# Kernel optimization log

Measured on AMD Instinct MI355X. Metric: run time of the kernel, lower is better.

The kernel has to match this reference:

```python
import jax, jax.numpy as jnp
import numpy as np

N, E = 20000, 160000
NFEAT, NHID, NCLASS = 512, 256, 64


def _unif(key, shape):
    s = 1.0 / np.sqrt(shape[-1])
    return jax.random.uniform(key, shape, jnp.float32, -s, s)


def setup_inputs() -> dict:
    key = jax.random.key(0)
    ks = jax.random.split(key, 16)
    return {
        "x": jax.random.normal(ks[0], (N, NFEAT), jnp.float32),
        "edge_index": jax.random.randint(ks[1], (2, E), 0, N, dtype=jnp.int32).astype(jnp.int64),
        "head": 0,
        # Relation 1 (nfeat -> nfeat)
        "r1_g1": _unif(ks[2], (NFEAT, NFEAT)),
        "r1_g2": _unif(ks[3], (NFEAT, NFEAT)),
        "r1_b1": _unif(ks[4], (NFEAT, NFEAT)),
        "r1_b2": _unif(ks[5], (NFEAT, NFEAT)),
        "r1_m": _unif(ks[6], (1, NFEAT)),
        "gc1_w": _unif(ks[7], (NHID, NFEAT)),   # GCNConv.lin.weight [out,in]
        "gc1_b": jnp.zeros((NHID,), jnp.float32),
        # Relation 2 (nhid -> nhid)
        "r2_g1": _unif(ks[8], (NHID, NHID)),
        "r2_g2": _unif(ks[9], (NHID, NHID)),
        "r2_b1": _unif(ks[10], (NHID, NHID)),
        "r2_b2": _unif(ks[11], (NHID, NHID)),
        "r2_m": _unif(ks[12], (1, NHID)),
        "gc2_w": _unif(ks[13], (NCLASS, NHID)),
        "gc2_b": jnp.zeros((NCLASS,), jnp.float32),
    }


def _scatter_mean(vals, idx, n):
    s = jax.ops.segment_sum(vals, idx, num_segments=n)
    c = jax.ops.segment_sum(jnp.ones(idx.shape, vals.dtype), idx, num_segments=n)
    return s / jnp.clip(c, 1.0)[:, None]


def _relation(ft, nb, g1, g2, b1, b2, m):
    # gamma/beta FiLM-style modulation, then TransE-style translation
    gamma = jax.nn.leaky_relu(ft @ g1.T + nb @ g2.T, 0.2) + 1.0
    beta = jax.nn.leaky_relu(ft @ b1.T + nb @ b2.T, 0.2)
    return ft + (gamma * m + beta) - nb


def _gcn(x, edge_index, w, b):
    # PyG GCNConv with add_self_loops=True, symmetric normalization
    n = x.shape[0]
    h = x @ w.T
    loop = jnp.arange(n, dtype=edge_index.dtype)
    row = jnp.concatenate([edge_index[0], loop])
    col = jnp.concatenate([edge_index[1], loop])
    deg = jax.ops.segment_sum(jnp.ones(col.shape, h.dtype), col, num_segments=n)
    dinv = jnp.where(deg > 0, deg ** -0.5, 0.0)
    norm = dinv[row] * dinv[col]
    out = jax.ops.segment_sum(norm[:, None] * h[row], col, num_segments=n)
    return out + b


def _trans_gcn(x, edge_index, rg1, rg2, rb1, rb2, rm, gw, gb, head):
    row, col = edge_index[0], edge_index[1]
    n = x.shape[0]
    num_nb = jax.ops.segment_sum(jnp.ones(row.shape, x.dtype), row, num_segments=n)
    nb = _scatter_mean(x[col], row, n)
    output = _relation(x, nb, rg1, rg2, rb1, rb2, rm)
    h_k = _gcn(x, edge_index, gw, gb)
    if not head:  # tail branch (ablation=0: h_s = output)
        h_s = output @ gw.T
        h_k = (h_k + h_s) / (num_nb + 1.0)[:, None]
    return h_k, output


def reference(x, edge_index, head, r1_g1, r1_g2, r1_b1, r1_b2, r1_m, gc1_w, gc1_b,
              r2_g1, r2_g2, r2_b1, r2_b2, r2_m, gc2_w, gc2_b):
    x1, out1 = _trans_gcn(x, edge_index, r1_g1, r1_g2, r1_b1, r1_b2, r1_m, gc1_w, gc1_b, head)
    x1 = jax.nn.elu(x1)  # dropout is identity in eval mode
    x2, out2 = _trans_gcn(x1, edge_index, r2_g1, r2_g2, r2_b1, r2_b2, r2_m, gc2_w, gc2_b, head)
    return (x2, jax.nn.log_softmax(x2, axis=1), out1, out2)
```

## Files before the change

### kernel.cpp

```cpp
#include <hip/hip_runtime.h>
#include <hip/hip_bf16.h>
#include <stdint.h>

typedef __bf16 bf16;
typedef __attribute__((ext_vector_type(8))) __bf16 bf16x8;
typedef __attribute__((ext_vector_type(4))) float f32x4;

#define NNODE 20000
#define NEDGE 160000
#define NFEATD 512
#define NHIDD 256
#define NCLSD 64

__device__ __forceinline__ void async_copy16(const bf16* g, bf16* l) {
  __builtin_amdgcn_global_load_lds((__attribute__((address_space(1))) void*)g,
                                   (__attribute__((address_space(3))) void*)l,
                                   16, 0, 0);
}

struct GemmArgs {
  const bf16 *A1, *A2, *W1, *W2, *zpage;
  int ldA, ldW, K1, Ktot, Nvalid, ldC, Nrows, Arows, Wrows;
  bf16* outB;
  float* outF;
  float* outF2;
  const float* mrow;
  const float* Xf;
  const bf16* Xh;
  const bf16* nbm;
  float* outG;
  bf16* outB2;
  const float* agg;
  const bf16* hself;
  int hld;
  const float* dinv;
  const float* bias;
  const float* rnb;
  int elu;
};

template <int MODE>
__global__ __launch_bounds__(256) void gemm_bt(GemmArgs ga) {
  __shared__ bf16 sA[2][128 * 64];
  __shared__ bf16 sB[2][128 * 64];
  const int tid = threadIdx.x;
  const int lane = tid & 63;
  const int w = tid >> 6;
  const int wm = w >> 1, wn = w & 1;

  const int gx = gridDim.x;
  const int nwg = gx * gridDim.y;
  const int orig = blockIdx.y * gx + blockIdx.x;
  const int qq = nwg >> 3, rm = nwg & 7;
  const int xcd = orig & 7, sidx = orig >> 3;
  const int wg = (xcd < rm ? xcd * (qq + 1) : rm * (qq + 1) + (xcd - rm) * qq) + sidx;
  const int bn0 = (wg % gx) * 128;
  const int bm0 = (wg / gx) * 128;

  const int srow = tid >> 3;
  const int scol = (((tid & 7) ^ (srow & 7)) << 3);
  const bf16* zp = ga.zpage + tid * 8;
  int offA[4], offB[4];
  bool okA[4], okB[4];
#pragma unroll
  for (int r = 0; r < 4; r++) {
    const int ra = bm0 + r * 32 + srow;
    const int rb = bn0 + r * 32 + srow;
    okA[r] = ra < ga.Arows;
    okB[r] = rb < ga.Wrows;
    offA[r] = ra * ga.ldA + scol;
    offB[r] = rb * ga.ldW + scol;
  }
  const int nt1 = ga.K1 >> 6;
  const int nt = ga.Ktot >> 6;

  auto stage = [&](int t, int p) {
    const int seg = t >= nt1;
    const int koff = (t - (seg ? nt1 : 0)) << 6;
    const bf16* As = seg ? ga.A2 : ga.A1;
    const bf16* Ws = seg ? ga.W2 : ga.W1;
    bf16* dA = &sA[p][tid * 8];
    bf16* dB = &sB[p][tid * 8];
#pragma unroll
    for (int r = 0; r < 4; r++)
      async_copy16(okA[r] ? As + offA[r] + koff : zp, dA + r * 2048);
#pragma unroll
    for (int r = 0; r < 4; r++)
      async_copy16(okB[r] ? Ws + offB[r] + koff : zp, dB + r * 2048);
  };

  const int sl = lane >> 4;
  const int rAb = wm * 64 + (lane & 15);
  const int rBb = wn * 64 + (lane & 15);
  const int a7 = rAb & 7, b7 = rBb & 7;

  f32x4 acc[4][4] = {};

  stage(0, 0);
  stage(1, 1);
  asm volatile("s_waitcnt vmcnt(8)" ::: "memory");
  __builtin_amdgcn_s_barrier();
  asm volatile("" ::: "memory");

  for (int t = 0; t < nt; ++t) {
    const int p = t & 1;
    const bf16* pA = &sA[p][0];
    const bf16* pB = &sB[p][0];
    bf16x8 af[4][2], bv[4][2];
#pragma unroll
    for (int mi = 0; mi < 4; mi++)
#pragma unroll
      for (int kk = 0; kk < 2; kk++)
        af[mi][kk] = *(const bf16x8*)((const char*)pA + (rAb + mi * 16) * 128 +
                                      ((((kk << 2) + sl) ^ a7) << 4));
#pragma unroll
    for (int ni = 0; ni < 4; ni++)
#pragma unroll
      for (int kk = 0; kk < 2; kk++)
        bv[ni][kk] = *(const bf16x8*)((const char*)pB + (rBb + ni * 16) * 128 +
                                      ((((kk << 2) + sl) ^ b7) << 4));
    if (t + 2 < nt) {
      asm volatile("s_waitcnt lgkmcnt(0)" ::: "memory");
      __builtin_amdgcn_s_barrier();
      asm volatile("" ::: "memory");
      stage(t + 2, p);
    }
    __builtin_amdgcn_s_setprio(1);
#pragma unroll
    for (int mi = 0; mi < 4; mi++)
#pragma unroll
      for (int ni = 0; ni < 4; ni++)
#pragma unroll
        for (int kk = 0; kk < 2; kk++)
          acc[mi][ni] =
              __builtin_amdgcn_mfma_f32_16x16x32_bf16(af[mi][kk], bv[ni][kk], acc[mi][ni], 0, 0, 0);
    __builtin_amdgcn_s_setprio(0);
    if (t + 1 < nt) {
      if (t + 2 < nt) asm volatile("s_waitcnt vmcnt(8)" ::: "memory");
      else            asm volatile("s_waitcnt vmcnt(0)" ::: "memory");
      __builtin_amdgcn_s_barrier();
      asm volatile("" ::: "memory");
    }
  }

  if constexpr (MODE == 0) {
    const int Nv = ga.Nvalid;
#pragma unroll
    for (int mi = 0; mi < 4; mi++) {
      const int rb = bm0 + wm * 64 + mi * 16 + ((lane >> 4) << 2);
#pragma unroll
      for (int ni = 0; ni < 4; ni++) {
        const int c = bn0 + wn * 64 + ni * 16 + (lane & 15);
#pragma unroll
        for (int i = 0; i < 4; i++) {
          const int r = rb + i;
          if (r < ga.Nrows && c < Nv) ga.outB[(size_t)r * ga.ldC + c] = (bf16)acc[mi][ni][i];
        }
      }
    }
  } else if constexpr (MODE == 2) {
    const int Dr = ga.Nvalid;
    const int Lb = ((bn0 + wn * 64) >> 1) + (lane & 15);
#pragma unroll
    for (int mi = 0; mi < 4; mi++) {
      const int rb = bm0 + wm * 64 + mi * 16 + ((lane >> 4) << 2);
#pragma unroll
      for (int p = 0; p < 2; p++) {
        const int L = Lb + p * 16;
        const float mv = ga.mrow[L];
#pragma unroll
        for (int i = 0; i < 4; i++) {
          const int r = rb + i;
          if (r >= ga.Nrows) continue;
          const size_t idx = (size_t)r * Dr + L;
          float vg = acc[mi][2 * p][i];
          float vb = acc[mi][2 * p + 1][i];
          float gamma = (vg > 0.f ? vg : 0.2f * vg) + 1.0f;
          float beta = vb > 0.f ? vb : 0.2f * vb;
          float ft = ga.Xf ? ga.Xf[idx] : (float)ga.Xh[idx];
          float o = ft + gamma * mv + beta - (float)ga.nbm[idx];
          ga.outG[idx] = o;
          ga.outB2[idx] = (bf16)o;
        }
      }
    }
  } else if constexpr (MODE == 3) {
    const int Nv = ga.Nvalid;
#pragma unroll
    for (int mi = 0; mi < 4; mi++) {
      const int rb = bm0 + wm * 64 + mi * 16 + ((lane >> 4) << 2);
#pragma unroll
      for (int ni = 0; ni < 4; ni++) {
        const int c = bn0 + wn * 64 + ni * 16 + (lane & 15);
#pragma unroll
        for (int i = 0; i < 4; i++) {
          const int r = rb + i;
          if (r >= ga.Nrows || c >= Nv) continue;
          const size_t idx = (size_t)r * ga.ldC + c;
          float dv = ga.dinv[r];
          float hs = (float)ga.hself[(size_t)r * ga.hld + c];
          float hv = (ga.agg[idx] + dv * dv * hs + ga.bias[c] + acc[mi][ni][i]) * ga.rnb[r];
          if (ga.elu) hv = hv > 0.f ? hv : expm1f(hv);
          ga.outB[idx] = (bf16)hv;
        }
      }
    }
  } else {
    if (wn == 0) {
#pragma unroll
      for (int mi = 0; mi < 4; mi++) {
        const int rb = bm0 + wm * 64 + mi * 16 + ((lane >> 4) << 2);
#pragma unroll
        for (int i = 0; i < 4; i++) {
          const int r = rb + i;
          const bool ok = r < ga.Nrows;
          float dv = ok ? ga.dinv[r] : 0.f;
          float rn = ok ? ga.rnb[r] : 1.f;
          float hv[4];
#pragma unroll
          for (int ni = 0; ni < 4; ni++) {
            const int c = ni * 16 + (lane & 15);
            float hs = ok ? (float)ga.hself[(size_t)r * ga.hld + c] : 0.f;
            float ag = ok ? ga.agg[(size_t)r * 64 + c] : 0.f;
            hv[ni] = ok ? (ag + dv * dv * hs + ga.bias[c] + acc[mi][ni][i]) * rn : 0.f;
          }
          float mx = fmaxf(fmaxf(hv[0], hv[1]), fmaxf(hv[2], hv[3]));
          mx = fmaxf(mx, __shfl_xor(mx, 1));
          mx = fmaxf(mx, __shfl_xor(mx, 2));
          mx = fmaxf(mx, __shfl_xor(mx, 4));
          mx = fmaxf(mx, __shfl_xor(mx, 8));
          float s = expf(hv[0] - mx) + expf(hv[1] - mx) + expf(hv[2] - mx) + expf(hv[3] - mx);
          s += __shfl_xor(s, 1);
          s += __shfl_xor(s, 2);
          s += __shfl_xor(s, 4);
          s += __shfl_xor(s, 8);
          float ls = logf(s);
          if (ok) {
#pragma unroll
            for (int ni = 0; ni < 4; ni++) {
              const int c = ni * 16 + (lane & 15);
              ga.outF[(size_t)r * 64 + c] = hv[ni];
              ga.outF2[(size_t)r * 64 + c] = hv[ni] - mx - ls;
            }
          }
        }
      }
    }
  }
}

__global__ void cvt_f2b(const float* __restrict__ src, bf16* __restrict__ dst, int n) {
  int i = (blockIdx.x * 256 + threadIdx.x) * 4;
  if (i >= n) return;
  float4 v = *(const float4*)(src + i);
  dst[i + 0] = (bf16)v.x;
  dst[i + 1] = (bf16)v.y;
  dst[i + 2] = (bf16)v.z;
  dst[i + 3] = (bf16)v.w;
}

__global__ void build_rel_w(const float* __restrict__ g1, const float* __restrict__ g2,
                            const float* __restrict__ b1, const float* __restrict__ b2,
                            bf16* __restrict__ dst, int D) {
  int idx = (blockIdx.x * 256 + threadIdx.x) * 4;
  if (idx >= 4 * D * D) return;
  int R = idx / (2 * D), C = idx % (2 * D);
  int q = R >> 5, s = R & 31;
  int sr = q * 16 + (s & 15);
  const float* src = (s < 16) ? ((C < D) ? g1 : g2) : ((C < D) ? b1 : b2);
  int cc = (C < D) ? C : C - D;
  float4 v = *(const float4*)(src + (size_t)sr * D + cc);
  union { bf16 b[4]; uint2 u; } o;
  o.b[0] = (bf16)v.x; o.b[1] = (bf16)v.y; o.b[2] = (bf16)v.z; o.b[3] = (bf16)v.w;
  *(uint2*)(dst + (size_t)R * 2 * D + C) = o.u;
}

__global__ void count_int(const int* __restrict__ ei, int* cr, int* cc, int E) {
  int e = blockIdx.x * 256 + threadIdx.x;
  if (e < E) {
    atomicAdd(&cr[ei[e]], 1);
    atomicAdd(&cc[ei[E + e]], 1);
  }
}

__global__ void scan_excl2(const int* __restrict__ cr, const int* __restrict__ cc,
                           int* __restrict__ rptr, int* __restrict__ cptr,
                           int* __restrict__ curr, int* __restrict__ curc, int n) {
  const int* cnt = blockIdx.x ? cc : cr;
  int* ptr = blockIdx.x ? cptr : rptr;
  int* cur = blockIdx.x ? curc : curr;
  __shared__ int part[256];
  int t = threadIdx.x;
  int chunk = (n + 255) / 256;
  int base = t * chunk;
  int s = 0;
  for (int i = 0; i < chunk; i++) {
    int j = base + i;
    if (j < n) s += cnt[j];
  }
  part[t] = s;
  __syncthreads();
  if (t == 0) {
    int r = 0;
    for (int i = 0; i < 256; i++) { int v = part[i]; part[i] = r; r += v; }
    ptr[n] = r;
  }
  __syncthreads();
  int run = part[t];
  for (int i = 0; i < chunk; i++) {
    int j = base + i;
    if (j < n) {
      ptr[j] = run;
      cur[j] = run;
      run += cnt[j];
    }
  }
}

__global__ void csr_fill(const int* __restrict__ ei, int* cur_r, int* cur_c,
                         int* __restrict__ adj_r, int* __restrict__ adj_c, int E) {
  int e = blockIdx.x * 256 + threadIdx.x;
  if (e >= E) return;
  int row = ei[e], col = ei[E + e];
  int p = atomicAdd(&cur_r[row], 1);
  adj_r[p] = col;
  int q = atomicAdd(&cur_c[col], 1);
  adj_c[q] = row;
}

__global__ void finalize_counts_i(const int* __restrict__ cr, const int* __restrict__ cc,
                                  float* nbscale, float* rnb, float* dinv, int n) {
  int i = blockIdx.x * 256 + threadIdx.x;
  if (i < n) {
    float a = (float)cr[i];
    nbscale[i] = 1.0f / fmaxf(a, 1.0f);
    rnb[i] = 1.0f / (a + 1.0f);
    dinv[i] = rsqrtf((float)cc[i] + 1.0f);
  }
}

__global__ void spmm_nb1(const int* __restrict__ rowptr, const int* __restrict__ adj,
                         const bf16* __restrict__ x, const float* __restrict__ nbscale,
                         bf16* __restrict__ nbp, int n) {
  int r = blockIdx.x * 4 + (threadIdx.x >> 6);
  if (r >= n) return;
  int lane = threadIdx.x & 63;
  int e0 = rowptr[r], e1 = rowptr[r + 1];
  float a[8] = {0.f, 0.f, 0.f, 0.f, 0.f, 0.f, 0.f, 0.f};
  for (int e = e0; e < e1; e++) {
    union { uint4 u; bf16 b[8]; } v;
    v.u = *(const uint4*)(x + (size_t)adj[e] * NFEATD + lane * 8);
#pragma unroll
    for (int j = 0; j < 8; j++) a[j] += (float)v.b[j];
  }
  float s = nbscale[r];
  union { bf16 b[8]; uint4 u; } o;
#pragma unroll
  for (int j = 0; j < 8; j++) o.b[j] = (bf16)(a[j] * s);
  *(uint4*)(nbp + (size_t)r * NFEATD + lane * 8) = o.u;
}

__global__ void spmm_nb2(const int* __restrict__ rowptr, const int* __restrict__ adj,
                         const bf16* __restrict__ x, const float* __restrict__ nbscale,
                         bf16* __restrict__ nbp, int n) {
  int r = blockIdx.x * 4 + (threadIdx.x >> 6);
  if (r >= n) return;
  int lane = threadIdx.x & 63;
  int e0 = rowptr[r], e1 = rowptr[r + 1];
  float a[4] = {0.f, 0.f, 0.f, 0.f};
  for (int e = e0; e < e1; e++) {
    union { uint2 u; bf16 b[4]; } v;
    v.u = *(const uint2*)(x + (size_t)adj[e] * NHIDD + lane * 4);
#pragma unroll
    for (int j = 0; j < 4; j++) a[j] += (float)v.b[j];
  }
  float s = nbscale[r];
  union { bf16 b[4]; uint2 u; } o;
#pragma unroll
  for (int j = 0; j < 4; j++) o.b[j] = (bf16)(a[j] * s);
  *(uint2*)(nbp + (size_t)r * NHIDD + lane * 4) = o.u;
}

__global__ void spmm_gcn256(const int* __restrict__ colptr, const int* __restrict__ adj,
                            const bf16* __restrict__ h, int hld, const float* __restrict__ dinv,
                            float* __restrict__ agg, int n) {
  int c = blockIdx.x * 4 + (threadIdx.x >> 6);
  if (c >= n) return;
  int lane = threadIdx.x & 63;
  int e0 = colptr[c], e1 = colptr[c + 1];
  float a[4] = {0.f, 0.f, 0.f, 0.f};
  for (int e = e0; e < e1; e++) {
    int rr = adj[e];
    float wv = dinv[rr];
    union { uint2 u; bf16 b[4]; } v;
    v.u = *(const uint2*)(h + (size_t)rr * hld + lane * 4);
#pragma unroll
    for (int j = 0; j < 4; j++) a[j] += wv * (float)v.b[j];
  }
  float wc = dinv[c];
  f32x4 o;
#pragma unroll
  for (int j = 0; j < 4; j++) o[j] = a[j] * wc;
  *(f32x4*)(agg + (size_t)c * NHIDD + lane * 4) = o;
}

__global__ void spmm_gcn64(const int* __restrict__ colptr, const int* __restrict__ adj,
                           const bf16* __restrict__ h, int hld, const float* __restrict__ dinv,
                           float* __restrict__ agg, int n) {
  int c = blockIdx.x * 4 + (threadIdx.x >> 6);
  if (c >= n) return;
  int lane = threadIdx.x & 63;
  int e0 = colptr[c], e1 = colptr[c + 1];
  float a = 0.f;
  for (int e = e0; e < e1; e++) {
    int rr = adj[e];
    a += dinv[rr] * (float)h[(size_t)rr * hld + lane];
  }
  agg[(size_t)c * NCLSD + lane] = a * dinv[c];
}

extern "C" void kernel_launch(void* const* d_in, const int* in_sizes, int n_in, void* d_out,
                              int out_size, void* d_ws, size_t ws_size, hipStream_t stream) {
  const float* x = (const float*)d_in[0];
  const int* ei = (const int*)d_in[1];
  const float* r1g1 = (const float*)d_in[3];
  const float* r1g2 = (const float*)d_in[4];
  const float* r1b1 = (const float*)d_in[5];
  const float* r1b2 = (const float*)d_in[6];
  const float* r1m = (const float*)d_in[7];
  const float* gc1w = (const float*)d_in[8];
  const float* gc1b = (const float*)d_in[9];
  const float* r2g1 = (const float*)d_in[10];
  const float* r2g2 = (const float*)d_in[11];
  const float* r2b1 = (const float*)d_in[12];
  const float* r2b2 = (const float*)d_in[13];
  const float* r2m = (const float*)d_in[14];
  const float* gc2w = (const float*)d_in[15];
  const float* gc2b = (const float*)d_in[16];
  float* out = (float*)d_out;

  char* ws = (char*)d_ws;
  size_t off = 0;
  auto alloc = [&](size_t bytes) -> char* {
    char* p = ws + off;
    off = (off + bytes + 511) & ~(size_t)511;
    return p;
  };
  float* nbscale = (float*)alloc((size_t)NNODE * 4);
  float* rnb = (float*)alloc((size_t)NNODE * 4);
  float* dinv = (float*)alloc((size_t)NNODE * 4);
  int* icr = (int*)alloc((size_t)NNODE * 4);
  int* icc = (int*)alloc((size_t)NNODE * 4);
  int* rptr = (int*)alloc((size_t)(NNODE + 1) * 4);
  int* cptr = (int*)alloc((size_t)(NNODE + 1) * 4);
  int* curr = (int*)alloc((size_t)NNODE * 4);
  int* curc = (int*)alloc((size_t)NNODE * 4);
  int* adjr = (int*)alloc((size_t)NEDGE * 4);
  int* adjc = (int*)alloc((size_t)NEDGE * 4);
  bf16* zpage = (bf16*)alloc(8192);
  bf16* Wrel1 = (bf16*)alloc((size_t)1024 * 1024 * 2);
  bf16* Wrel2 = (bf16*)alloc((size_t)512 * 512 * 2);
  bf16* wgc1 = (bf16*)alloc((size_t)NHIDD * NFEATD * 2);
  bf16* wgc2 = (bf16*)alloc((size_t)NCLSD * NHIDD * 2);
  bf16* xb = (bf16*)alloc((size_t)NNODE * NFEATD * 2);
  bf16* nbp1 = (bf16*)alloc((size_t)NNODE * NFEATD * 2);
  bf16* out1b = (bf16*)alloc((size_t)NNODE * NFEATD * 2);
  bf16* h1b = (bf16*)alloc((size_t)NNODE * NHIDD * 2);
  float* agg1 = (float*)alloc((size_t)NNODE * NHIDD * 4);
  bf16* x1b = (bf16*)alloc((size_t)NNODE * NHIDD * 2);
  bf16* nb2p = (bf16*)alloc((size_t)NNODE * NHIDD * 2);
  bf16* out2b = (bf16*)alloc((size_t)NNODE * NHIDD * 2);
  bf16* h2b = (bf16*)alloc((size_t)NNODE * NCLSD * 2);
  float* agg2 = (float*)alloc((size_t)NNODE * NCLSD * 4);

  const size_t OUT1OFF = (size_t)2 * NNODE * NCLSD;
  const size_t OUT2OFF = OUT1OFF + (size_t)NNODE * NFEATD;
  float* out1g = out + OUT1OFF;
  float* out2g = out + OUT2OFF;

  const int MB = (NNODE + 127) / 128;
  const int NW4 = (NNODE + 3) / 4;

  hipMemsetAsync(icr, 0, (size_t)NNODE * 4, stream);
  hipMemsetAsync(icc, 0, (size_t)NNODE * 4, stream);
  hipMemsetAsync(zpage, 0, 8192, stream);
  count_int<<<(NEDGE + 255) / 256, 256, 0, stream>>>(ei, icr, icc, NEDGE);
  scan_excl2<<<2, 256, 0, stream>>>(icr, icc, rptr, cptr, curr, curc, NNODE);
  finalize_counts_i<<<(NNODE + 255) / 256, 256, 0, stream>>>(icr, icc, nbscale, rnb, dinv, NNODE);
  csr_fill<<<(NEDGE + 255) / 256, 256, 0, stream>>>(ei, curr, curc, adjr, adjc, NEDGE);

  cvt_f2b<<<(NNODE * NFEATD / 4 + 255) / 256, 256, 0, stream>>>(x, xb, NNODE * NFEATD);
  cvt_f2b<<<(NHIDD * NFEATD / 4 + 255) / 256, 256, 0, stream>>>(gc1w, wgc1, NHIDD * NFEATD);
  cvt_f2b<<<(NCLSD * NHIDD / 4 + 255) / 256, 256, 0, stream>>>(gc2w, wgc2, NCLSD * NHIDD);
  build_rel_w<<<(4 * 512 * 512 / 4 + 255) / 256, 256, 0, stream>>>(r1g1, r1g2, r1b1, r1b2, Wrel1, 512);
  build_rel_w<<<(4 * 256 * 256 / 4 + 255) / 256, 256, 0, stream>>>(r2g1, r2g2, r2b1, r2b2, Wrel2, 256);

  spmm_nb1<<<NW4, 256, 0, stream>>>(rptr, adjr, xb, nbscale, nbp1, NNODE);

  GemmArgs a;
  auto base = [&](const bf16* A1, const bf16* A2, int ldA, const bf16* W1, const bf16* W2,
                  int ldW, int K1, int Kt, int Nv, int ldC, int Wr) {
    a = GemmArgs{};
    a.A1 = A1; a.A2 = A2; a.W1 = W1; a.W2 = W2; a.zpage = zpage;
    a.ldA = ldA; a.ldW = ldW; a.K1 = K1; a.Ktot = Kt; a.Nvalid = Nv; a.ldC = ldC;
    a.Nrows = NNODE; a.Arows = NNODE; a.Wrows = Wr;
  };

  base(xb, nbp1, NFEATD, Wrel1, Wrel1 + 512, 1024, NFEATD, 2 * NFEATD, NFEATD, NFEATD, 1024);
  a.mrow = r1m; a.Xf = x; a.nbm = nbp1; a.outG = out1g; a.outB2 = out1b;
  gemm_bt<2><<<dim3(8, MB), 256, 0, stream>>>(a);

  base(xb, xb, NFEATD, wgc1, wgc1, NFEATD, NFEATD, NFEATD, NHIDD, NHIDD, NHIDD);
  a.outB = h1b;
  gemm_bt<0><<<dim3(2, MB), 256, 0, stream>>>(a);

  spmm_gcn256<<<NW4, 256, 0, stream>>>(cptr, adjc, h1b, NHIDD, dinv, agg1, NNODE);

  base(out1b, out1b, NFEATD, wgc1, wgc1, NFEATD, NFEATD, NFEATD, NHIDD, NHIDD, NHIDD);
  a.agg = agg1; a.hself = h1b; a.hld = NHIDD; a.dinv = dinv; a.bias = gc1b; a.rnb = rnb;
  a.elu = 1; a.outB = x1b;
  gemm_bt<3><<<dim3(2, MB), 256, 0, stream>>>(a);

  spmm_nb2<<<NW4, 256, 0, stream>>>(rptr, adjr, x1b, nbscale, nb2p, NNODE);

  base(x1b, nb2p, NHIDD, Wrel2, Wrel2 + 256, 512, NHIDD, 2 * NHIDD, NHIDD, NHIDD, 512);
  a.mrow = r2m; a.Xf = nullptr; a.Xh = x1b; a.nbm = nb2p; a.outG = out2g; a.outB2 = out2b;
  gemm_bt<2><<<dim3(4, MB), 256, 0, stream>>>(a);

  base(x1b, x1b, NHIDD, wgc2, wgc2, NHIDD, NHIDD, NHIDD, NCLSD, NCLSD, NCLSD);
  a.outB = h2b;
  gemm_bt<0><<<dim3(1, MB), 256, 0, stream>>>(a);

  spmm_gcn64<<<NW4, 256, 0, stream>>>(cptr, adjc, h2b, NCLSD, dinv, agg2, NNODE);

  base(out2b, out2b, NHIDD, wgc2, wgc2, NHIDD, NHIDD, NHIDD, NCLSD, NCLSD, NCLSD);
  a.agg = agg2; a.hself = h2b; a.hld = NCLSD; a.dinv = dinv; a.bias = gc2b; a.rnb = rnb;
  a.elu = 0; a.outF = out; a.outF2 = out + (size_t)NNODE * NCLSD;
  gemm_bt<4><<<dim3(1, MB), 256, 0, stream>>>(a);
}
```

Before: 534.7 us.

## Switch GEMM to triple-buffered 32-wide K tiles with one barrier per step

The bf16 MFMA GEMM now stages K in 32-element tiles across three LDS buffers instead of 64-element tiles across two, with a new XOR swizzle matching the 64-byte row pitch. Each iteration now has one barrier instead of two, and the next load is issued after the compute, keeping two tiles in flight. LDS use drops, which could allow more resident workgroups. In exchange there are twice as many iterations and barriers, and fewer MFMAs per barrier.

```diff
diff --git a/kernel.cpp b/kernel.cpp
--- a/kernel.cpp
+++ b/kernel.cpp
@@ -41,8 +41,8 @@
 
 template <int MODE>
 __global__ __launch_bounds__(256) void gemm_bt(GemmArgs ga) {
-  __shared__ bf16 sA[2][128 * 64];
-  __shared__ bf16 sB[2][128 * 64];
+  __shared__ bf16 sA[3][128 * 32];
+  __shared__ bf16 sB[3][128 * 32];
   const int tid = threadIdx.x;
   const int lane = tid & 63;
   const int w = tid >> 6;
@@ -57,90 +57,78 @@
   const int bn0 = (wg % gx) * 128;
   const int bm0 = (wg / gx) * 128;
 
-  const int srow = tid >> 3;
-  const int scol = (((tid & 7) ^ (srow & 7)) << 3);
+  const int srow = tid >> 2;
+  const int scol = (((tid & 3) ^ ((srow >> 1) & 3)) << 3);
   const bf16* zp = ga.zpage + tid * 8;
-  int offA[4], offB[4];
-  bool okA[4], okB[4];
-#pragma unroll
-  for (int r = 0; r < 4; r++) {
-    const int ra = bm0 + r * 32 + srow;
-    const int rb = bn0 + r * 32 + srow;
+  int offA[2], offB[2];
+  bool okA[2], okB[2];
+#pragma unroll
+  for (int r = 0; r < 2; r++) {
+    const int ra = bm0 + r * 64 + srow;
+    const int rb = bn0 + r * 64 + srow;
     okA[r] = ra < ga.Arows;
     okB[r] = rb < ga.Wrows;
     offA[r] = ra * ga.ldA + scol;
     offB[r] = rb * ga.ldW + scol;
   }
-  const int nt1 = ga.K1 >> 6;
-  const int nt = ga.Ktot >> 6;
-
-  auto stage = [&](int t, int p) {
+  const int nt1 = ga.K1 >> 5;
+  const int nt = ga.Ktot >> 5;
+
+  auto stage = [&](int t, int b) {
     const int seg = t >= nt1;
-    const int koff = (t - (seg ? nt1 : 0)) << 6;
+    const int koff = (t - (seg ? nt1 : 0)) << 5;
     const bf16* As = seg ? ga.A2 : ga.A1;
     const bf16* Ws = seg ? ga.W2 : ga.W1;
-    bf16* dA = &sA[p][tid * 8];
-    bf16* dB = &sB[p][tid * 8];
-#pragma unroll
-    for (int r = 0; r < 4; r++)
-      async_copy16(okA[r] ? As + offA[r] + koff : zp, dA + r * 2048);
-#pragma unroll
-    for (int r = 0; r < 4; r++)
-      async_copy16(okB[r] ? Ws + offB[r] + koff : zp, dB + r * 2048);
+#pragma unroll
+    for (int r = 0; r < 2; r++)
+      async_copy16(okA[r] ? As + offA[r] + koff : zp, &sA[b][r * 2048 + tid * 8]);
+#pragma unroll
+    for (int r = 0; r < 2; r++)
+      async_copy16(okB[r] ? Ws + offB[r] + koff : zp, &sB[b][r * 2048 + tid * 8]);
   };
 
-  const int sl = lane >> 4;
   const int rAb = wm * 64 + (lane & 15);
   const int rBb = wn * 64 + (lane & 15);
-  const int a7 = rAb & 7, b7 = rBb & 7;
+  const int s3 = ((lane & 15) >> 1) & 3;
+  const int apos = (((lane >> 4) ^ s3) << 4);
 
   f32x4 acc[4][4] = {};
 
   stage(0, 0);
   stage(1, 1);
+  stage(2, 2);
   asm volatile("s_waitcnt vmcnt(8)" ::: "memory");
   __builtin_amdgcn_s_barrier();
   asm volatile("" ::: "memory");
 
+  int b = 0;
   for (int t = 0; t < nt; ++t) {
-    const int p = t & 1;
-    const bf16* pA = &sA[p][0];
-    const bf16* pB = &sB[p][0];
-    bf16x8 af[4][2], bv[4][2];
+    const bf16* pA = &sA[b][0];
+    const bf16* pB = &sB[b][0];
+    bf16x8 af[4], bv[4];
 #pragma unroll
     for (int mi = 0; mi < 4; mi++)
-#pragma unroll
-      for (int kk = 0; kk < 2; kk++)
-        af[mi][kk] = *(const bf16x8*)((const char*)pA + (rAb + mi * 16) * 128 +
-                                      ((((kk << 2) + sl) ^ a7) << 4));
+      af[mi] = *(const bf16x8*)((const char*)pA + (rAb + mi * 16) * 64 + apos);
 #pragma unroll
     for (int ni = 0; ni < 4; ni++)
-#pragma unroll
-      for (int kk = 0; kk < 2; kk++)
-        bv[ni][kk] = *(const bf16x8*)((const char*)pB + (rBb + ni * 16) * 128 +
-                                      ((((kk << 2) + sl) ^ b7) << 4));
-    if (t + 2 < nt) {
-      asm volatile("s_waitcnt lgkmcnt(0)" ::: "memory");
-      __builtin_amdgcn_s_barrier();
-      asm volatile("" ::: "memory");
-      stage(t + 2, p);
-    }
+      bv[ni] = *(const bf16x8*)((const char*)pB + (rBb + ni * 16) * 64 + apos);
     __builtin_amdgcn_s_setprio(1);
 #pragma unroll
     for (int mi = 0; mi < 4; mi++)
 #pragma unroll
       for (int ni = 0; ni < 4; ni++)
-#pragma unroll
-        for (int kk = 0; kk < 2; kk++)
-          acc[mi][ni] =
-              __builtin_amdgcn_mfma_f32_16x16x32_bf16(af[mi][kk], bv[ni][kk], acc[mi][ni], 0, 0, 0);
+        acc[mi][ni] =
+            __builtin_amdgcn_mfma_f32_16x16x32_bf16(af[mi], bv[ni], acc[mi][ni], 0, 0, 0);
     __builtin_amdgcn_s_setprio(0);
     if (t + 1 < nt) {
-      if (t + 2 < nt) asm volatile("s_waitcnt vmcnt(8)" ::: "memory");
+      asm volatile("s_waitcnt lgkmcnt(0)" ::: "memory");
+      if (t + 2 < nt) asm volatile("s_waitcnt vmcnt(4)" ::: "memory");
       else            asm volatile("s_waitcnt vmcnt(0)" ::: "memory");
       __builtin_amdgcn_s_barrier();
       asm volatile("" ::: "memory");
+      if (t + 3 < nt) stage(t + 3, b);
     }
+    b = (b == 2) ? 0 : b + 1;
   }
 
   if constexpr (MODE == 0) {
```

Result: slower. 570.8 us (+6.8%).

## Fuse GCN linear GEMMs into relation GEMM launches and unroll SpMM edge loops

Applied to the files above, without the earlier changes.

The GCN projection GEMM (x@W^T) is merged into the relation GEMM launch as extra N-tiles. Blocks past the relation's column range switch to the GCN weight and K and write bf16 h directly, which removes two kernel launches and lets the two GEMMs share one grid. Separately, all four SpMM gather kernels unroll their edge loops by four to issue more independent loads per iteration. The cost is extra branching and register pressure in the MODE 2 kernel, plus load imbalance between tiles with different K lengths in the same grid.

```diff
diff --git a/kernel.cpp b/kernel.cpp
--- a/kernel.cpp
+++ b/kernel.cpp
@@ -37,6 +37,8 @@
   const float* bias;
   const float* rnb;
   int elu;
+  const bf16* Wh;
+  int ldWh, Wrowsh, Kh, Nintmain;
 };
 
 template <int MODE>
@@ -57,6 +59,15 @@
   const int bn0 = (wg % gx) * 128;
   const int bm0 = (wg / gx) * 128;
 
+  const bool isH = (MODE == 2) && ga.Wh && (bn0 >= ga.Nintmain);
+  const bf16* Wp1 = isH ? ga.Wh : ga.W1;
+  const bf16* Wp2 = isH ? ga.Wh : ga.W2;
+  const int ldW = isH ? ga.ldWh : ga.ldW;
+  const int Wrows = isH ? ga.Wrowsh : ga.Wrows;
+  const int bn0L = isH ? bn0 - ga.Nintmain : bn0;
+  const int nt1 = (isH ? ga.Kh : ga.K1) >> 6;
+  const int nt = (isH ? ga.Kh : ga.Ktot) >> 6;
+
   const int srow = tid >> 3;
   const int scol = (((tid & 7) ^ (srow & 7)) << 3);
   const bf16* zp = ga.zpage + tid * 8;
@@ -65,20 +76,18 @@
 #pragma unroll
   for (int r = 0; r < 4; r++) {
     const int ra = bm0 + r * 32 + srow;
-    const int rb = bn0 + r * 32 + srow;
+    const int rb = bn0L + r * 32 + srow;
     okA[r] = ra < ga.Arows;
-    okB[r] = rb < ga.Wrows;
+    okB[r] = rb < Wrows;
     offA[r] = ra * ga.ldA + scol;
-    offB[r] = rb * ga.ldW + scol;
-  }
-  const int nt1 = ga.K1 >> 6;
-  const int nt = ga.Ktot >> 6;
+    offB[r] = rb * ldW + scol;
+  }
 
   auto stage = [&](int t, int p) {
     const int seg = t >= nt1;
     const int koff = (t - (seg ? nt1 : 0)) << 6;
     const bf16* As = seg ? ga.A2 : ga.A1;
-    const bf16* Ws = seg ? ga.W2 : ga.W1;
+    const bf16* Ws = seg ? Wp2 : Wp1;
     bf16* dA = &sA[p][tid * 8];
     bf16* dB = &sB[p][tid * 8];
 #pragma unroll
@@ -159,28 +168,44 @@
       }
     }
   } else if constexpr (MODE == 2) {
-    const int Dr = ga.Nvalid;
-    const int Lb = ((bn0 + wn * 64) >> 1) + (lane & 15);
-#pragma unroll
-    for (int mi = 0; mi < 4; mi++) {
-      const int rb = bm0 + wm * 64 + mi * 16 + ((lane >> 4) << 2);
-#pragma unroll
-      for (int p = 0; p < 2; p++) {
-        const int L = Lb + p * 16;
-        const float mv = ga.mrow[L];
-#pragma unroll
-        for (int i = 0; i < 4; i++) {
-          const int r = rb + i;
-          if (r >= ga.Nrows) continue;
-          const size_t idx = (size_t)r * Dr + L;
-          float vg = acc[mi][2 * p][i];
-          float vb = acc[mi][2 * p + 1][i];
-          float gamma = (vg > 0.f ? vg : 0.2f * vg) + 1.0f;
-          float beta = vb > 0.f ? vb : 0.2f * vb;
-          float ft = ga.Xf ? ga.Xf[idx] : (float)ga.Xh[idx];
-          float o = ft + gamma * mv + beta - (float)ga.nbm[idx];
-          ga.outG[idx] = o;
-          ga.outB2[idx] = (bf16)o;
+    if (isH) {
+#pragma unroll
+      for (int mi = 0; mi < 4; mi++) {
+        const int rb = bm0 + wm * 64 + mi * 16 + ((lane >> 4) << 2);
+#pragma unroll
+        for (int ni = 0; ni < 4; ni++) {
+          const int c = bn0L + wn * 64 + ni * 16 + (lane & 15);
+#pragma unroll
+          for (int i = 0; i < 4; i++) {
+            const int r = rb + i;
+            if (r < ga.Nrows && c < ga.ldC) ga.outB[(size_t)r * ga.ldC + c] = (bf16)acc[mi][ni][i];
+          }
+        }
+      }
+    } else {
+      const int Dr = ga.Nvalid;
+      const int Lb = ((bn0 + wn * 64) >> 1) + (lane & 15);
+#pragma unroll
+      for (int mi = 0; mi < 4; mi++) {
+        const int rb = bm0 + wm * 64 + mi * 16 + ((lane >> 4) << 2);
+#pragma unroll
+        for (int p = 0; p < 2; p++) {
+          const int L = Lb + p * 16;
+          const float mv = ga.mrow[L];
+#pragma unroll
+          for (int i = 0; i < 4; i++) {
+            const int r = rb + i;
+            if (r >= ga.Nrows) continue;
+            const size_t idx = (size_t)r * Dr + L;
+            float vg = acc[mi][2 * p][i];
+            float vb = acc[mi][2 * p + 1][i];
+            float gamma = (vg > 0.f ? vg : 0.2f * vg) + 1.0f;
+            float beta = vb > 0.f ? vb : 0.2f * vb;
+            float ft = ga.Xf ? ga.Xf[idx] : (float)ga.Xh[idx];
+            float o = ft + gamma * mv + beta - (float)ga.nbm[idx];
+            ga.outG[idx] = o;
+            ga.outB2[idx] = (bf16)o;
+          }
         }
       }
     }
@@ -347,7 +372,19 @@
   int lane = threadIdx.x & 63;
   int e0 = rowptr[r], e1 = rowptr[r + 1];
   float a[8] = {0.f, 0.f, 0.f, 0.f, 0.f, 0.f, 0.f, 0.f};
-  for (int e = e0; e < e1; e++) {
+  int e = e0;
+  for (; e + 4 <= e1; e += 4) {
+    int i0 = adj[e], i1 = adj[e + 1], i2 = adj[e + 2], i3 = adj[e + 3];
+    union { uint4 u; bf16 b[8]; } v0, v1, v2, v3;
+    v0.u = *(const uint4*)(x + (size_t)i0 * NFEATD + lane * 8);
+    v1.u = *(const uint4*)(x + (size_t)i1 * NFEATD + lane * 8);
+    v2.u = *(const uint4*)(x + (size_t)i2 * NFEATD + lane * 8);
+    v3.u = *(const uint4*)(x + (size_t)i3 * NFEATD + lane * 8);
+#pragma unroll
+    for (int j = 0; j < 8; j++)
+      a[j] += (float)v0.b[j] + (float)v1.b[j] + (float)v2.b[j] + (float)v3.b[j];
+  }
+  for (; e < e1; e++) {
     union { uint4 u; bf16 b[8]; } v;
     v.u = *(const uint4*)(x + (size_t)adj[e] * NFEATD + lane * 8);
 #pragma unroll
@@ -368,7 +405,19 @@
   int lane = threadIdx.x & 63;
   int e0 = rowptr[r], e1 = rowptr[r + 1];
   float a[4] = {0.f, 0.f, 0.f, 0.f};
-  for (int e = e0; e < e1; e++) {
+  int e = e0;
+  for (; e + 4 <= e1; e += 4) {
+    int i0 = adj[e], i1 = adj[e + 1], i2 = adj[e + 2], i3 = adj[e + 3];
+    union { uint2 u; bf16 b[4]; } v0, v1, v2, v3;
+    v0.u = *(const uint2*)(x + (size_t)i0 * NHIDD + lane * 4);
+    v1.u = *(const uint2*)(x + (size_t)i1 * NHIDD + lane * 4);
+    v2.u = *(const uint2*)(x + (size_t)i2 * NHIDD + lane * 4);
+    v3.u = *(const uint2*)(x + (size_t)i3 * NHIDD + lane * 4);
+#pragma unroll
+    for (int j = 0; j < 4; j++)
+      a[j] += (float)v0.b[j] + (float)v1.b[j] + (float)v2.b[j] + (float)v3.b[j];
+  }
+  for (; e < e1; e++) {
     union { uint2 u; bf16 b[4]; } v;
     v.u = *(const uint2*)(x + (size_t)adj[e] * NHIDD + lane * 4);
 #pragma unroll
@@ -389,7 +438,20 @@
   int lane = threadIdx.x & 63;
   int e0 = colptr[c], e1 = colptr[c + 1];
   float a[4] = {0.f, 0.f, 0.f, 0.f};
-  for (int e = e0; e < e1; e++) {
+  int e = e0;
+  for (; e + 4 <= e1; e += 4) {
+    int i0 = adj[e], i1 = adj[e + 1], i2 = adj[e + 2], i3 = adj[e + 3];
+    float w0 = dinv[i0], w1 = dinv[i1], w2 = dinv[i2], w3 = dinv[i3];
+    union { uint2 u; bf16 b[4]; } v0, v1, v2, v3;
+    v0.u = *(const uint2*)(h + (size_t)i0 * hld + lane * 4);
+    v1.u = *(const uint2*)(h + (size_t)i1 * hld + lane * 4);
+    v2.u = *(const uint2*)(h + (size_t)i2 * hld + lane * 4);
+    v3.u = *(const uint2*)(h + (size_t)i3 * hld + lane * 4);
+#pragma unroll
+    for (int j = 0; j < 4; j++)
+      a[j] += w0 * (float)v0.b[j] + w1 * (float)v1.b[j] + w2 * (float)v2.b[j] + w3 * (float)v3.b[j];
+  }
+  for (; e < e1; e++) {
     int rr = adj[e];
     float wv = dinv[rr];
     union { uint2 u; bf16 b[4]; } v;
@@ -412,7 +474,16 @@
   int lane = threadIdx.x & 63;
   int e0 = colptr[c], e1 = colptr[c + 1];
   float a = 0.f;
-  for (int e = e0; e < e1; e++) {
+  int e = e0;
+  for (; e + 4 <= e1; e += 4) {
+    int i0 = adj[e], i1 = adj[e + 1], i2 = adj[e + 2], i3 = adj[e + 3];
+    float h0 = (float)h[(size_t)i0 * hld + lane];
+    float h1 = (float)h[(size_t)i1 * hld + lane];
+    float h2 = (float)h[(size_t)i2 * hld + lane];
+    float h3 = (float)h[(size_t)i3 * hld + lane];
+    a += dinv[i0] * h0 + dinv[i1] * h1 + dinv[i2] * h2 + dinv[i3] * h3;
+  }
+  for (; e < e1; e++) {
     int rr = adj[e];
     a += dinv[rr] * (float)h[(size_t)rr * hld + lane];
   }
@@ -506,13 +577,11 @@
     a.Nrows = NNODE; a.Arows = NNODE; a.Wrows = Wr;
   };
 
-  base(xb, nbp1, NFEATD, Wrel1, Wrel1 + 512, 1024, NFEATD, 2 * NFEATD, NFEATD, NFEATD, 1024);
+  base(xb, nbp1, NFEATD, Wrel1, Wrel1 + 512, 1024, NFEATD, 2 * NFEATD, NFEATD, NHIDD, 1024);
   a.mrow = r1m; a.Xf = x; a.nbm = nbp1; a.outG = out1g; a.outB2 = out1b;
-  gemm_bt<2><<<dim3(8, MB), 256, 0, stream>>>(a);
-
-  base(xb, xb, NFEATD, wgc1, wgc1, NFEATD, NFEATD, NFEATD, NHIDD, NHIDD, NHIDD);
+  a.Wh = wgc1; a.ldWh = NFEATD; a.Wrowsh = NHIDD; a.Kh = NFEATD; a.Nintmain = 1024;
   a.outB = h1b;
-  gemm_bt<0><<<dim3(2, MB), 256, 0, stream>>>(a);
+  gemm_bt<2><<<dim3(10, MB), 256, 0, stream>>>(a);
 
   spmm_gcn256<<<NW4, 256, 0, stream>>>(cptr, adjc, h1b, NHIDD, dinv, agg1, NNODE);
 
@@ -523,13 +592,11 @@
 
   spmm_nb2<<<NW4, 256, 0, stream>>>(rptr, adjr, x1b, nbscale, nb2p, NNODE);
 
-  base(x1b, nb2p, NHIDD, Wrel2, Wrel2 + 256, 512, NHIDD, 2 * NHIDD, NHIDD, NHIDD, 512);
+  base(x1b, nb2p, NHIDD, Wrel2, Wrel2 + 256, 512, NHIDD, 2 * NHIDD, NHIDD, NCLSD, 512);
   a.mrow = r2m; a.Xf = nullptr; a.Xh = x1b; a.nbm = nb2p; a.outG = out2g; a.outB2 = out2b;
-  gemm_bt<2><<<dim3(4, MB), 256, 0, stream>>>(a);
-
-  base(x1b, x1b, NHIDD, wgc2, wgc2, NHIDD, NHIDD, NHIDD, NCLSD, NCLSD, NCLSD);
+  a.Wh = wgc2; a.ldWh = NHIDD; a.Wrowsh = NCLSD; a.Kh = NHIDD; a.Nintmain = 512;
   a.outB = h2b;
-  gemm_bt<0><<<dim3(1, MB), 256, 0, stream>>>(a);
+  gemm_bt<2><<<dim3(5, MB), 256, 0, stream>>>(a);
 
   spmm_gcn64<<<NW4, 256, 0, stream>>>(cptr, adjc, h2b, NCLSD, dinv, agg2, NNODE);
 
```

After: 495.8 us. 1.08x faster.
